# Kernel optimization log

Measured on AMD Instinct MI355X. Metric: run time of the kernel, lower is better.

Reference implementation:

```python
import jax, jax.numpy as jnp
import numpy as np

DT = 0.01          # Euler step size
ALPHA = 1.0        # Grubb exponent (hardcoded in forward())
V0 = 0.02          # resting venous blood volume fraction
NOISE_AMP = 0.01   # amplitude of per-step noise injected into the neural drive
T = 1000           # integration length (hardcoded in forward())
B = 16384          # batch of independent simulations


def setup_inputs() -> dict:
    key = jax.random.key(0)
    noise = jax.random.normal(key, (T, B), dtype=jnp.float32)
    f32 = lambda v: jnp.asarray(v, dtype=jnp.float32)
    return {
        "noise": noise,
        "sigma": f32(0.9),
        "mu": f32(0.8),
        "lamb": f32(0.3),
        "beta": f32(0.9),
        "psi": f32(0.5),
        "phi": f32(2.0),
        "chi": f32(0.3),
    }


def reference(noise, sigma, mu, lamb, beta, psi, phi, chi):
    # Balloon-Windkessel BOLD model, explicit Euler, per-step noise.
    # States per simulation: s (vasodilatory signal), f (flow), v (volume), q (dHb).
    b = noise.shape[1]
    inv_alpha = 1.0 / ALPHA

    def step(carry, z):
        s, f, v, q = carry
        # oxygen extraction fraction E(f) = 1 - (1 - E0)^(1/f)
        E = 1.0 - (1.0 - beta) ** (1.0 / f)
        v_a = v ** inv_alpha  # outflow v^(1/alpha)
        s2 = s + DT * (NOISE_AMP * z - sigma * s - mu * (f - 1.0))
        f2 = f + DT * s
        v2 = v + DT * (f - v_a) / lamb
        q2 = q + DT * (f * E / beta - v_a * q / v) / lamb
        # BOLD readout at the new state
        y = V0 * (phi * (1.0 - q2) + psi * (1.0 - q2 / v2) + chi * (1.0 - v2))
        return (s2, f2, v2, q2), y

    init = (
        jnp.zeros((b,), noise.dtype),
        jnp.ones((b,), noise.dtype),
        jnp.ones((b,), noise.dtype),
        jnp.ones((b,), noise.dtype),
    )
    _, ys = jax.lax.scan(step, init, noise)  # ys: [T, B]
    return ys
```

## Files before the change

kernel.cpp:

```cpp
#include <hip/hip_runtime.h>


#define BATCH     16384
#define DT        0.01f
#define NOISE_AMP 0.01f
#define V0        0.02f
#define CHUNKS    20
#define CL        50
#define GSIMS     32
#define NTHREADS  (CHUNKS * GSIMS)

#if __has_builtin(__builtin_amdgcn_exp2f)
#define EXP2F(x) __builtin_amdgcn_exp2f(x)
#else
#define EXP2F(x) exp2f(x)
#endif

__device__ __forceinline__ float uf(float x) {
    return __uint_as_float(__builtin_amdgcn_readfirstlane(__float_as_uint(x)));
}

struct D22 { double a, b, c, d; };
__device__ __forceinline__ D22 dmul(D22 x, D22 y) {
    D22 r;
    r.a = x.a * y.a + x.b * y.c;  r.b = x.a * y.b + x.b * y.d;
    r.c = x.c * y.a + x.d * y.c;  r.d = x.c * y.b + x.d * y.d;
    return r;
}

__global__ __launch_bounds__(NTHREADS, 5) void balloon_scan(
    const float* __restrict__ noise,
    const float* __restrict__ p_sigma,
    const float* __restrict__ p_mu,
    const float* __restrict__ p_lamb,
    const float* __restrict__ p_beta,
    const float* __restrict__ p_psi,
    const float* __restrict__ p_phi,
    const float* __restrict__ p_chi,
    float* __restrict__ out)
{
    const int tid = threadIdx.x;
    const int g   = tid & (GSIMS - 1);
    const int cc  = tid >> 5;
    const int sim = blockIdx.x * GSIMS + g;

    const float sigma = uf(p_sigma[0]);
    const float mu    = uf(p_mu[0]);
    const float lamb  = uf(p_lamb[0]);
    const float beta  = uf(p_beta[0]);
    const float psi   = uf(p_psi[0]);
    const float phi   = uf(p_phi[0]);
    const float chi   = uf(p_chi[0]);

    const float as_   = 1.0f - DT * sigma;
    const float dtn   = DT * NOISE_AMP;
    const float dtm   = DT * mu;
    const float dt_il = uf((float)(0.01 / (double)lamb));
    const float av    = 1.0f - dt_il;
    const float kq    = uf(dt_il / beta);
    const float lc    = uf(log2f(1.0f - beta));
    const float c0 = V0 * (phi + psi + chi), c1 = V0 * phi, c2 = V0 * psi, c3 = V0 * chi;

    D22 A; A.a = 1.0 - 0.01 * (double)sigma; A.b = -0.01 * (double)mu;
           A.c = 0.01;                       A.d = 1.0;
    D22 A2 = dmul(A, A), A4 = dmul(A2, A2), A8 = dmul(A4, A4);
    D22 A16 = dmul(A8, A8), A32 = dmul(A16, A16);
    D22 P = dmul(dmul(A32, A16), A2);
    double avd = 1.0 - 0.01 / (double)lamb;
    double av2 = avd * avd, av4 = av2 * av2, av8 = av4 * av4;
    double av16 = av8 * av8, av32 = av16 * av16;
    double ap = av32 * av16 * av2;

    float M11[5], M12[5], M21[5], M22[5], AVP[5];
#pragma unroll
    for (int j = 0; j < 5; ++j) {
        M11[j] = uf((float)P.a); M12[j] = uf((float)P.b);
        M21[j] = uf((float)P.c); M22[j] = uf((float)P.d);
        AVP[j] = uf((float)ap);
        P = dmul(P, P); ap = ap * ap;
    }

    float ws = 0.0f, wf = 1.0f, avc = 1.0f;
#pragma unroll
    for (int j = 0; j < 5; ++j) {
        if ((cc >> j) & 1) {
            float t = __builtin_fmaf(M11[j], ws, M12[j] * wf);
            wf = __builtin_fmaf(M21[j], ws, M22[j] * wf);
            ws = t;
            avc *= AVP[j];
        }
    }

    __shared__ float sA[NTHREADS];
    __shared__ float sB[NTHREADS];

    const float* zp = noise + cc * (CL * BATCH) + sim;

    float rs = 0.0f, rf = 0.0f;
#pragma unroll 10
    for (int j = 0; j < CL; ++j) {
        const float z = zp[j * BATCH];
        const float u = __builtin_fmaf(dtn, z, dtm);
        const float t = __builtin_fmaf(as_, rs, __builtin_fmaf(-dtm, rf, u));
        rf = __builtin_fmaf(DT, rs, rf);
        rs = t;
    }

    sA[tid] = rs; sB[tid] = rf;
    __syncthreads();
#pragma unroll
    for (int j = 0; j < 5; ++j) {
        const int off = 1 << j;
        float ns = 0.0f, nf = 0.0f;
        const bool has = (cc >= off);
        if (has) { ns = sA[tid - off * GSIMS]; nf = sB[tid - off * GSIMS]; }
        __syncthreads();
        if (has) {
            rs = __builtin_fmaf(M11[j], ns, __builtin_fmaf(M12[j], nf, rs));
            rf = __builtin_fmaf(M21[j], ns, __builtin_fmaf(M22[j], nf, rf));
            sA[tid] = rs; sB[tid] = rf;
        }
        __syncthreads();
    }
    float s0 = ws, f0 = wf;
    if (cc > 0) { s0 += sA[tid - GSIMS]; f0 += sB[tid - GSIMS]; }
    __syncthreads();

    float s = s0, f = f0, Rv = 0.0f, Rq = 0.0f;
#pragma unroll 10
    for (int j = 0; j < CL; ++j) {
        const float z    = zp[j * BATCH];
        const float invf = __builtin_amdgcn_rcpf(f);
        const float e2   = EXP2F(lc * invf);
        const float t1   = __builtin_fmaf(-f, e2, f);
        Rv = __builtin_fmaf(av, Rv, dt_il * f);
        Rq = __builtin_fmaf(av, Rq, kq * t1);
        const float s2 = __builtin_fmaf(as_, s,
                         __builtin_fmaf(dtn, z,
                         __builtin_fmaf(-dtm, f, dtm)));
        f = __builtin_fmaf(DT, s, f);
        s = s2;
    }

    sA[tid] = Rv; sB[tid] = Rq;
    __syncthreads();
#pragma unroll
    for (int j = 0; j < 5; ++j) {
        const int off = 1 << j;
        float nv = 0.0f, nq = 0.0f;
        const bool has = (cc >= off);
        if (has) { nv = sA[tid - off * GSIMS]; nq = sB[tid - off * GSIMS]; }
        __syncthreads();
        if (has) {
            Rv = __builtin_fmaf(AVP[j], nv, Rv);
            Rq = __builtin_fmaf(AVP[j], nq, Rq);
            sA[tid] = Rv; sB[tid] = Rq;
        }
        __syncthreads();
    }
    float v = avc, q = avc;
    if (cc > 0) { v += sA[tid - GSIMS]; q += sB[tid - GSIMS]; }

    s = s0; f = f0;
    float* op = out + cc * (CL * BATCH) + sim;
#pragma unroll 10
    for (int j = 0; j < CL; ++j) {
        const float z    = zp[j * BATCH];
        const float invf = __builtin_amdgcn_rcpf(f);
        const float e2   = EXP2F(lc * invf);
        const float t1   = __builtin_fmaf(-f, e2, f);
        const float vn   = __builtin_fmaf(av, v, dt_il * f);
        const float qn   = __builtin_fmaf(av, q, kq * t1);
        const float s2 = __builtin_fmaf(as_, s,
                         __builtin_fmaf(dtn, z,
                         __builtin_fmaf(-dtm, f, dtm)));
        f = __builtin_fmaf(DT, s, f);
        s = s2;

        const float invv = __builtin_amdgcn_rcpf(vn);
        const float y = __builtin_fmaf(-c2, qn * invv,
                        __builtin_fmaf(-c3, vn,
                        __builtin_fmaf(-c1, qn, c0)));
        op[j * BATCH] = y;
        v = vn; q = qn;
    }
}

extern "C" void kernel_launch(void* const* d_in, const int* in_sizes, int n_in,
                              void* d_out, int out_size, void* d_ws, size_t ws_size,
                              hipStream_t stream) {
    const float* noise   = (const float*)d_in[0];
    const float* p_sigma = (const float*)d_in[1];
    const float* p_mu    = (const float*)d_in[2];
    const float* p_lamb  = (const float*)d_in[3];
    const float* p_beta  = (const float*)d_in[4];
    const float* p_psi   = (const float*)d_in[5];
    const float* p_phi   = (const float*)d_in[6];
    const float* p_chi   = (const float*)d_in[7];

    balloon_scan<<<BATCH / GSIMS, NTHREADS, 0, stream>>>(
        noise, p_sigma, p_mu, p_lamb, p_beta, p_psi, p_phi, p_chi,
        (float*)d_out);
}
```

Measured before the change: 142.9 us.

## Process two sims per thread with float2 loads, cache noise in registers, finer chunks

Each thread now handles two adjacent simulations using 8-byte vector loads and stores. The time axis is split into 40 chunks of 25 steps instead of 20 of 50, with a 6-level scan. Noise for the whole chunk is kept in registers, so it is read from global memory once instead of three times. Outputs use nontemporal stores and the scan exchanges one float4 per thread through shared memory. The cost is higher register pressure from the 25 cached float2 values, which may reduce occupancy below the launch-bounds target, plus one extra scan level.

```diff
diff --git a/kernel.cpp b/kernel.cpp
--- a/kernel.cpp
+++ b/kernel.cpp
@@ -1,14 +1,18 @@
 #include <hip/hip_runtime.h>
 
 
-#define BATCH     16384
-#define DT        0.01f
+#define BATCH    16384
+#define ROW2     (BATCH / 2)
+#define DT       0.01f
 #define NOISE_AMP 0.01f
-#define V0        0.02f
-#define CHUNKS    20
-#define CL        50
-#define GSIMS     32
-#define NTHREADS  (CHUNKS * GSIMS)
+#define V0       0.02f
+#define CHUNKS   40
+#define CL       25
+#define LPR      16
+#define NTHREADS (CHUNKS * LPR)
+#define SCAND    6
+
+typedef float v2f __attribute__((ext_vector_type(2)));
 
 #if __has_builtin(__builtin_amdgcn_exp2f)
 #define EXP2F(x) __builtin_amdgcn_exp2f(x)
@@ -39,10 +43,9 @@
     const float* __restrict__ p_chi,
     float* __restrict__ out)
 {
-    const int tid = threadIdx.x;
-    const int g   = tid & (GSIMS - 1);
-    const int cc  = tid >> 5;
-    const int sim = blockIdx.x * GSIMS + g;
+    const int tid  = threadIdx.x;
+    const int lane = tid & (LPR - 1);
+    const int cc   = tid >> 4;
 
     const float sigma = uf(p_sigma[0]);
     const float mu    = uf(p_mu[0]);
@@ -63,17 +66,15 @@
 
     D22 A; A.a = 1.0 - 0.01 * (double)sigma; A.b = -0.01 * (double)mu;
            A.c = 0.01;                       A.d = 1.0;
-    D22 A2 = dmul(A, A), A4 = dmul(A2, A2), A8 = dmul(A4, A4);
-    D22 A16 = dmul(A8, A8), A32 = dmul(A16, A16);
-    D22 P = dmul(dmul(A32, A16), A2);
+    D22 A2 = dmul(A, A), A4 = dmul(A2, A2), A8 = dmul(A4, A4), A16 = dmul(A8, A8);
+    D22 P  = dmul(dmul(A16, A8), A);
     double avd = 1.0 - 0.01 / (double)lamb;
-    double av2 = avd * avd, av4 = av2 * av2, av8 = av4 * av4;
-    double av16 = av8 * av8, av32 = av16 * av16;
-    double ap = av32 * av16 * av2;
-
-    float M11[5], M12[5], M21[5], M22[5], AVP[5];
-#pragma unroll
-    for (int j = 0; j < 5; ++j) {
+    double av2 = avd * avd, av4 = av2 * av2, av8 = av4 * av4, av16 = av8 * av8;
+    double ap  = av16 * av8 * avd;
+
+    float M11[SCAND], M12[SCAND], M21[SCAND], M22[SCAND], AVP[SCAND];
+#pragma unroll
+    for (int j = 0; j < SCAND; ++j) {
         M11[j] = uf((float)P.a); M12[j] = uf((float)P.b);
         M21[j] = uf((float)P.c); M22[j] = uf((float)P.d);
         AVP[j] = uf((float)ap);
@@ -82,107 +83,120 @@
 
     float ws = 0.0f, wf = 1.0f, avc = 1.0f;
 #pragma unroll
-    for (int j = 0; j < 5; ++j) {
+    for (int j = 0; j < SCAND; ++j) {
         if ((cc >> j) & 1) {
-            float t = __builtin_fmaf(M11[j], ws, M12[j] * wf);
+            const float t = __builtin_fmaf(M11[j], ws, M12[j] * wf);
             wf = __builtin_fmaf(M21[j], ws, M22[j] * wf);
-            ws = t;
-            avc *= AVP[j];
+            ws = t; avc *= AVP[j];
         }
     }
 
-    __shared__ float sA[NTHREADS];
-    __shared__ float sB[NTHREADS];
-
-    const float* zp = noise + cc * (CL * BATCH) + sim;
-
-    float rs = 0.0f, rf = 0.0f;
-#pragma unroll 10
-    for (int j = 0; j < CL; ++j) {
-        const float z = zp[j * BATCH];
-        const float u = __builtin_fmaf(dtn, z, dtm);
-        const float t = __builtin_fmaf(as_, rs, __builtin_fmaf(-dtm, rf, u));
-        rf = __builtin_fmaf(DT, rs, rf);
-        rs = t;
-    }
-
-    sA[tid] = rs; sB[tid] = rf;
-    __syncthreads();
-#pragma unroll
-    for (int j = 0; j < 5; ++j) {
-        const int off = 1 << j;
-        float ns = 0.0f, nf = 0.0f;
-        const bool has = (cc >= off);
-        if (has) { ns = sA[tid - off * GSIMS]; nf = sB[tid - off * GSIMS]; }
-        __syncthreads();
-        if (has) {
-            rs = __builtin_fmaf(M11[j], ns, __builtin_fmaf(M12[j], nf, rs));
-            rf = __builtin_fmaf(M21[j], ns, __builtin_fmaf(M22[j], nf, rf));
-            sA[tid] = rs; sB[tid] = rf;
-        }
-        __syncthreads();
-    }
-    float s0 = ws, f0 = wf;
-    if (cc > 0) { s0 += sA[tid - GSIMS]; f0 += sB[tid - GSIMS]; }
-    __syncthreads();
-
-    float s = s0, f = f0, Rv = 0.0f, Rq = 0.0f;
-#pragma unroll 10
-    for (int j = 0; j < CL; ++j) {
-        const float z    = zp[j * BATCH];
-        const float invf = __builtin_amdgcn_rcpf(f);
-        const float e2   = EXP2F(lc * invf);
-        const float t1   = __builtin_fmaf(-f, e2, f);
-        Rv = __builtin_fmaf(av, Rv, dt_il * f);
-        Rq = __builtin_fmaf(av, Rq, kq * t1);
+    auto sfstep = [&](float& s, float& f, float zz) {
         const float s2 = __builtin_fmaf(as_, s,
-                         __builtin_fmaf(dtn, z,
+                         __builtin_fmaf(dtn, zz,
                          __builtin_fmaf(-dtm, f, dtm)));
         f = __builtin_fmaf(DT, s, f);
         s = s2;
-    }
-
-    sA[tid] = Rv; sB[tid] = Rq;
+    };
+    auto vqfwd = [&](float f_, float& accv, float& accq) {
+        const float invf = __builtin_amdgcn_rcpf(f_);
+        const float e2   = EXP2F(lc * invf);
+        const float t1   = __builtin_fmaf(-f_, e2, f_);
+        accv = __builtin_fmaf(av, accv, dt_il * f_);
+        accq = __builtin_fmaf(av, accq, kq * t1);
+    };
+
+    __shared__ float4 ssc[NTHREADS];
+
+    const v2f* zg = (const v2f*)noise + (cc * CL) * ROW2 + blockIdx.x * LPR + lane;
+    v2f z[CL];
+
+    float rs0 = 0.f, rf0 = 0.f, rs1 = 0.f, rf1 = 0.f;
+#pragma unroll
+    for (int j = 0; j < CL; ++j) {
+        z[j] = zg[j * ROW2];
+        sfstep(rs0, rf0, z[j].x);
+        sfstep(rs1, rf1, z[j].y);
+    }
+
+    ssc[tid] = make_float4(rs0, rf0, rs1, rf1);
     __syncthreads();
 #pragma unroll
-    for (int j = 0; j < 5; ++j) {
+    for (int j = 0; j < SCAND; ++j) {
         const int off = 1 << j;
-        float nv = 0.0f, nq = 0.0f;
         const bool has = (cc >= off);
-        if (has) { nv = sA[tid - off * GSIMS]; nq = sB[tid - off * GSIMS]; }
+        float4 n = make_float4(0.f, 0.f, 0.f, 0.f);
+        if (has) n = ssc[tid - off * LPR];
         __syncthreads();
         if (has) {
-            Rv = __builtin_fmaf(AVP[j], nv, Rv);
-            Rq = __builtin_fmaf(AVP[j], nq, Rq);
-            sA[tid] = Rv; sB[tid] = Rq;
+            rs0 = __builtin_fmaf(M11[j], n.x, __builtin_fmaf(M12[j], n.y, rs0));
+            rf0 = __builtin_fmaf(M21[j], n.x, __builtin_fmaf(M22[j], n.y, rf0));
+            rs1 = __builtin_fmaf(M11[j], n.z, __builtin_fmaf(M12[j], n.w, rs1));
+            rf1 = __builtin_fmaf(M21[j], n.z, __builtin_fmaf(M22[j], n.w, rf1));
+            ssc[tid] = make_float4(rs0, rf0, rs1, rf1);
         }
         __syncthreads();
     }
-    float v = avc, q = avc;
-    if (cc > 0) { v += sA[tid - GSIMS]; q += sB[tid - GSIMS]; }
-
-    s = s0; f = f0;
-    float* op = out + cc * (CL * BATCH) + sim;
-#pragma unroll 10
+    float s0a = ws, f0a = wf, s0b = ws, f0b = wf;
+    if (cc > 0) {
+        const float4 pr = ssc[tid - LPR];
+        s0a += pr.x; f0a += pr.y; s0b += pr.z; f0b += pr.w;
+    }
+    __syncthreads();
+
+    float sa = s0a, fa = f0a, sb = s0b, fb = f0b;
+    float Rv0 = 0.f, Rq0 = 0.f, Rv1 = 0.f, Rq1 = 0.f;
+#pragma unroll
     for (int j = 0; j < CL; ++j) {
-        const float z    = zp[j * BATCH];
-        const float invf = __builtin_amdgcn_rcpf(f);
-        const float e2   = EXP2F(lc * invf);
-        const float t1   = __builtin_fmaf(-f, e2, f);
-        const float vn   = __builtin_fmaf(av, v, dt_il * f);
-        const float qn   = __builtin_fmaf(av, q, kq * t1);
-        const float s2 = __builtin_fmaf(as_, s,
-                         __builtin_fmaf(dtn, z,
-                         __builtin_fmaf(-dtm, f, dtm)));
-        f = __builtin_fmaf(DT, s, f);
-        s = s2;
-
-        const float invv = __builtin_amdgcn_rcpf(vn);
-        const float y = __builtin_fmaf(-c2, qn * invv,
-                        __builtin_fmaf(-c3, vn,
-                        __builtin_fmaf(-c1, qn, c0)));
-        op[j * BATCH] = y;
-        v = vn; q = qn;
+        vqfwd(fa, Rv0, Rq0);
+        vqfwd(fb, Rv1, Rq1);
+        sfstep(sa, fa, z[j].x);
+        sfstep(sb, fb, z[j].y);
+    }
+
+    ssc[tid] = make_float4(Rv0, Rq0, Rv1, Rq1);
+    __syncthreads();
+#pragma unroll
+    for (int j = 0; j < SCAND; ++j) {
+        const int off = 1 << j;
+        const bool has = (cc >= off);
+        float4 n = make_float4(0.f, 0.f, 0.f, 0.f);
+        if (has) n = ssc[tid - off * LPR];
+        __syncthreads();
+        if (has) {
+            Rv0 = __builtin_fmaf(AVP[j], n.x, Rv0);
+            Rq0 = __builtin_fmaf(AVP[j], n.y, Rq0);
+            Rv1 = __builtin_fmaf(AVP[j], n.z, Rv1);
+            Rq1 = __builtin_fmaf(AVP[j], n.w, Rq1);
+            ssc[tid] = make_float4(Rv0, Rq0, Rv1, Rq1);
+        }
+        __syncthreads();
+    }
+    float va = avc, qa = avc, vb = avc, qb = avc;
+    if (cc > 0) {
+        const float4 pr = ssc[tid - LPR];
+        va += pr.x; qa += pr.y; vb += pr.z; qb += pr.w;
+    }
+
+    sa = s0a; fa = f0a; sb = s0b; fb = f0b;
+    v2f* og = (v2f*)out + (cc * CL) * ROW2 + blockIdx.x * LPR + lane;
+#pragma unroll
+    for (int j = 0; j < CL; ++j) {
+        vqfwd(fa, va, qa);
+        vqfwd(fb, vb, qb);
+        sfstep(sa, fa, z[j].x);
+        sfstep(sb, fb, z[j].y);
+
+        const float ia = __builtin_amdgcn_rcpf(va);
+        const float ib = __builtin_amdgcn_rcpf(vb);
+        v2f y2;
+        y2.x = __builtin_fmaf(-c2, qa * ia,
+               __builtin_fmaf(-c3, va,
+               __builtin_fmaf(-c1, qa, c0)));
+        y2.y = __builtin_fmaf(-c2, qb * ib,
+               __builtin_fmaf(-c3, vb,
+               __builtin_fmaf(-c1, qb, c0)));
+        __builtin_nontemporal_store(y2, og + j * ROW2);
     }
 }
 
@@ -198,7 +212,7 @@
     const float* p_phi   = (const float*)d_in[6];
     const float* p_chi   = (const float*)d_in[7];
 
-    balloon_scan<<<BATCH / GSIMS, NTHREADS, 0, stream>>>(
+    balloon_scan<<<BATCH / (2 * LPR), NTHREADS, 0, stream>>>(
         noise, p_sigma, p_mu, p_lamb, p_beta, p_psi, p_phi, p_chi,
         (float*)d_out);
 }
```

Result: slower. 159.9 us (+11.9%).
